# Kernel optimization log

Hardware: AMD Instinct MI355X
Metric: run time of the kernel (lower is better)

Reference implementation:

```python
import jax, jax.numpy as jnp
import numpy as np

H = 256   # d_model (SSM copies)
N = 32    # half state size (conjugate symmetry)
S = 256   # n_ssm (trainable copies); repeat = H//S = 1
R = 1     # low-rank correction rank
CCH = 32  # channels; must equal N for the final dC contraction
LMAX = 2048
BATCH = 2


def _r2c(x):
    return x[..., 0] + 1j * x[..., 1]


def setup_inputs() -> dict:
    key = jax.random.key(0)
    ks = jax.random.split(key, 8)
    # dt ~ loguniform(1e-3, 1e-1), standard S4 init
    log_dt = jnp.log(1e-3) + jax.random.uniform(ks[0], (H,), dtype=jnp.float32) * (jnp.log(1e-1) - jnp.log(1e-3))
    B_ri = 0.5 * jax.random.normal(ks[1], (1, S, N, 2), dtype=jnp.float32)
    P_ri = 0.5 * jax.random.normal(ks[2], (R, S, N, 2), dtype=jnp.float32)
    C_ri = 0.5 * jax.random.normal(ks[3], (CCH, H, N, 2), dtype=jnp.float32)
    # real_type='exp': w_real = -exp(inv_w_real) < 0 (stable poles)
    inv_w_real = 0.5 * jax.random.normal(ks[4], (S, N), dtype=jnp.float32)
    # HiPPO-style imaginary parts ~ pi * n, with small noise
    w_imag = jnp.pi * jnp.broadcast_to(jnp.arange(N, dtype=jnp.float32), (S, N)) + 0.01 * jax.random.normal(ks[5], (S, N), dtype=jnp.float32)
    dC = 0.1 * jax.random.normal(ks[6], (LMAX, H, N), dtype=jnp.float32)
    previous_decode = jax.random.normal(ks[7], (BATCH, H, LMAX), dtype=jnp.float32)
    return dict(log_dt=log_dt, B_ri=B_ri, P_ri=P_ri, C_ri=C_ri,
                inv_w_real=inv_w_real, w_imag=w_imag, dC=dC,
                previous_decode=previous_decode, L=LMAX)


def _ss_kernel(log_dt, B_ri, P_ri, C_ri, inv_w_real, w_imag, L):
    """NPLR SSM kernel K_L via Cauchy evaluation + rank-1 Woodbury + irfft. Returns (channels, H, L) real."""
    H_ = log_dt.shape[0]
    S_ = inv_w_real.shape[0]
    rep = H_ // S_
    dt = jnp.exp(log_dt)                              # (H,)
    B = _r2c(B_ri)                                    # (1, S, N)
    P = _r2c(P_ri)                                    # (R, S, N)
    C = _r2c(C_ri)                                    # (CCH, H, N)
    Q = jnp.conj(P)
    w = -jnp.exp(inv_w_real) + 1j * w_imag            # (S, N), real_type='exp'
    # FFT nodes (roots of unity) and bilinear-transformed nodes
    Lf = L // 2 + 1
    omega = jnp.exp((-2j * jnp.pi / L) * jnp.arange(Lf, dtype=jnp.float32))  # (Lf,)
    z = 2 * (1 - omega) / (1 + omega)                 # (Lf,)
    # broadcast S -> H ('r t n -> r (v t) n')
    B = jnp.tile(B, (1, rep, 1))                      # (1, H, N)
    P = jnp.tile(P, (1, rep, 1))                      # (R, H, N)
    Q = jnp.tile(Q, (1, rep, 1))
    w = jnp.tile(w, (rep, 1)) * dt[:, None]           # (H, N) : w * dt
    Bc = jnp.concatenate([B, P], axis=0)              # (1+R, H, N)
    Cc = jnp.concatenate([C, Q], axis=0)              # (CCH+R, H, N)
    v = Bc[:, None] * Cc[None]                        # (1+R, CCH+R, H, N)
    # conjugate-symmetric Cauchy kernel: sum_n v/(z-w) + conj(v)/(z-conj(w))
    cau_p = 1.0 / (z[None, None, :] - w[:, :, None])              # (H, N, Lf)
    cau_m = 1.0 / (z[None, None, :] - jnp.conj(w)[:, :, None])    # (H, N, Lf)
    r = jnp.einsum('ijhn,hnl->ijhl', v, cau_p) + jnp.einsum('ijhn,hnl->ijhl', jnp.conj(v), cau_m)
    r = r * dt[None, None, :, None]
    # rank-1 Woodbury correction
    k_f = r[:-1, :-1] - r[:-1, -1:] * r[-1:, :-1] / (1 + r[-1:, -1:])  # (1, CCH, H, Lf)
    k_f = k_f * 2 / (1 + omega)
    k = jnp.fft.irfft(k_f, n=L, axis=-1)              # (1, CCH, H, L) real
    return k[-1]                                      # (CCH, H, L)


def reference(log_dt, B_ri, P_ri, C_ri, inv_w_real, w_imag, dC, previous_decode, L):
    k = _ss_kernel(log_dt, B_ri, P_ri, C_ri, inv_w_real, w_imag, L)  # (CCH, H, L)
    # FFT convolution of previous_decode with the kernel (length-2L, linear conv)
    k_f = jnp.fft.rfft(k, n=2 * L, axis=-1)                          # (CCH, H, L+1)
    pd_f = jnp.fft.rfft(previous_decode, n=2 * L, axis=-1)           # (B, H, L+1)
    x_f = jnp.einsum('bhl,chl->bhcl', pd_f, k_f)                     # (B, H, CCH, L+1)
    x_pred = jnp.fft.irfft(x_f, n=2 * L, axis=-1)[..., :L]           # (B, H, CCH, L)
    out = jnp.einsum('bhnl,lhn->bhl', x_pred, dC)                    # (B, H, L)
    return out
```

## Files before the change

### kernel.cpp

```cpp
#include <hip/hip_runtime.h>
#include <math.h>

#define LF   1025

#define OFF_ZT   65536
#define OFF_KF   131072
#define OFF_PDF  67371008
#define OFF_DCT  84148224

__device__ __forceinline__ float2 cmulf(float2 a, float2 b){
    return make_float2(a.x*b.x - a.y*b.y, a.x*b.y + a.y*b.x);
}
__device__ __forceinline__ int pidx(int i){ return i + (i >> 4); }

__device__ __forceinline__ float2 twid(float r){
    float s, c;
    asm("v_sin_f32 %0, %1" : "=v"(s) : "v"(r));
    asm("v_cos_f32 %0, %1" : "=v"(c) : "v"(r));
    return make_float2(c, -s);
}

__global__ void initk(float4* __restrict__ ZT){
    int i = blockIdx.x*256 + threadIdx.x;
    if (i < LF){
        double th = (-2.0*M_PI) * (double)i / 2048.0;
        double cr = cos(th), ci = sin(th);
        double ar = 1.0 + cr, ai = ci;
        double den = ar*ar + ai*ai;
        double nr = 1.0 - cr, ni = -ci;
        double zr = 2.0*(nr*ar + ni*ai)/den;
        double zi = 2.0*(ni*ar - nr*ai)/den;
        ZT[i] = make_float4((float)zr, (float)zi, (float)(2.0*ar/den), (float)(-2.0*ai/den));
    }
}

__global__ void transpose_dC(const float* __restrict__ dC, float* __restrict__ DCT){
    __shared__ float tile[32][33];
    int hc0 = blockIdx.x*32;
    int l0  = blockIdx.y*32;
    int tx = threadIdx.x;
    for (int i = threadIdx.y; i < 32; i += 8)
        tile[i][tx] = dC[(size_t)(l0+i)*8192 + hc0 + tx];
    __syncthreads();
    for (int i = threadIdx.y; i < 32; i += 8)
        DCT[(size_t)(hc0+i)*2048 + l0 + tx] = tile[tx][i];
}

__global__ __launch_bounds__(256) void cauchy_k(
                         const float* __restrict__ log_dt, const float* __restrict__ B_ri,
                         const float* __restrict__ P_ri, const float* __restrict__ C_ri,
                         const float* __restrict__ ivw, const float* __restrict__ wimag,
                         const float4* __restrict__ ZT, float2* __restrict__ KF)
{
    const int h  = blockIdx.y;
    const int c0 = blockIdx.z * 8;
    const int l  = blockIdx.x*256 + (int)threadIdx.x;
    __shared__ float wre[32], wim[32], bre[32], bim[32], ppre[32], ppim[32];
    __shared__ float cre[8][32], cim[8][32];
    __shared__ float dt_sh;
    if (threadIdx.x < 32){
        int n = threadIdx.x;
        float dt = expf(log_dt[h]);
        wre[n] = -expf(ivw[h*32+n]) * dt;
        wim[n] = wimag[h*32+n] * dt;
        bre[n] = B_ri[(h*32+n)*2+0];
        bim[n] = B_ri[(h*32+n)*2+1];
        ppre[n] = P_ri[(h*32+n)*2+0];
        ppim[n] = P_ri[(h*32+n)*2+1];
        if (n == 0) dt_sh = dt;
    }
    {
        int i = threadIdx.x;
        int cc = i >> 5, n = i & 31;
        size_t base = (((size_t)(c0+cc)*256 + h)*32 + n)*2;
        cre[cc][n] = C_ri[base+0];
        cim[cc][n] = C_ri[base+1];
    }
    __syncthreads();
    if (l >= LF) return;

    float4 zt = ZT[l];
    const float zx = zt.x, zy = zt.y;
    float r0x[9], r0y[9], r1x[9], r1y[9];
    #pragma unroll
    for (int j=0;j<9;++j){ r0x[j]=0.f; r0y[j]=0.f; r1x[j]=0.f; r1y[j]=0.f; }

    #pragma unroll 1
    for (int n=0; n<32; ++n){
        float wr = wre[n], wi = wim[n];
        float dx = zx - wr;
        float dy = zy - wi;
        float ey = zy + wi;
        float ip = 1.0f/(dx*dx + dy*dy);
        float im = 1.0f/(dx*dx + ey*ey);
        float cpx = dx*ip, cpy = -dy*ip;
        float cmx = dx*im, cmy = -ey*im;
        float br = bre[n], bi = bim[n];
        float t0x = br*cpx - bi*cpy, t0y = br*cpy + bi*cpx;
        float t1x = br*cmx + bi*cmy, t1y = br*cmy - bi*cmx;
        float pr = ppre[n], pi = ppim[n];
        float t2x = pr*cpx - pi*cpy, t2y = pr*cpy + pi*cpx;
        float t3x = pr*cmx + pi*cmy, t3y = pr*cmy - pi*cmx;
        float u0 = t0x+t1x, v0 = t1y-t0y, s0 = t0y+t1y, q0 = t0x-t1x;
        float u1 = t2x+t3x, v1 = t3y-t2y, s1 = t2y+t3y, q1 = t2x-t3x;
        #pragma unroll
        for (int j=0;j<8;++j){
            float a = cre[j][n], b = cim[j][n];
            r0x[j] = fmaf(a,u0, fmaf(b,v0, r0x[j]));
            r0y[j] = fmaf(a,s0, fmaf(b,q0, r0y[j]));
            r1x[j] = fmaf(a,u1, fmaf(b,v1, r1x[j]));
            r1y[j] = fmaf(a,s1, fmaf(b,q1, r1y[j]));
        }
        r0x[8] = fmaf(pr,u0, fmaf(-pi,v0, r0x[8]));
        r0y[8] = fmaf(pr,s0, fmaf(-pi,q0, r0y[8]));
        r1x[8] = fmaf(pr,u1, fmaf(-pi,v1, r1x[8]));
        r1y[8] = fmaf(pr,s1, fmaf(-pi,q1, r1y[8]));
    }

    float dt = dt_sh;
    #pragma unroll
    for (int j=0;j<9;++j){ r0x[j]*=dt; r0y[j]*=dt; r1x[j]*=dt; r1y[j]*=dt; }
    float drr = 1.0f + r1x[8], dii = r1y[8];
    float idn = 1.0f/(drr*drr + dii*dii);
    float gx = (r0x[8]*drr + r0y[8]*dii)*idn;
    float gy = (r0y[8]*drr - r0x[8]*dii)*idn;
    float tfx = zt.z, tfy = zt.w;
    #pragma unroll
    for (int j=0;j<8;++j){
        float kr = r0x[j] - (gx*r1x[j] - gy*r1y[j]);
        float ki = r0y[j] - (gx*r1y[j] + gy*r1x[j]);
        KF[((size_t)((c0+j)*256+h))*1026 + l] = make_float2(kr*tfx - ki*tfy, kr*tfy + ki*tfx);
    }
}

template<bool INV>
__device__ __forceinline__ void bfly8(float2 v[8]){
    float2 e0,e1,e2,e3,o0,o1,o2,o3;
    {
        float t0x=v[0].x+v[4].x, t0y=v[0].y+v[4].y;
        float t1x=v[0].x-v[4].x, t1y=v[0].y-v[4].y;
        float t2x=v[2].x+v[6].x, t2y=v[2].y+v[6].y;
        float t3x=v[2].x-v[6].x, t3y=v[2].y-v[6].y;
        e0 = make_float2(t0x+t2x, t0y+t2y);
        e2 = make_float2(t0x-t2x, t0y-t2y);
        if (!INV){ e1 = make_float2(t1x+t3y, t1y-t3x); e3 = make_float2(t1x-t3y, t1y+t3x); }
        else     { e1 = make_float2(t1x-t3y, t1y+t3x); e3 = make_float2(t1x+t3y, t1y-t3x); }
    }
    {
        float t0x=v[1].x+v[5].x, t0y=v[1].y+v[5].y;
        float t1x=v[1].x-v[5].x, t1y=v[1].y-v[5].y;
        float t2x=v[3].x+v[7].x, t2y=v[3].y+v[7].y;
        float t3x=v[3].x-v[7].x, t3y=v[3].y-v[7].y;
        o0 = make_float2(t0x+t2x, t0y+t2y);
        o2 = make_float2(t0x-t2x, t0y-t2y);
        if (!INV){ o1 = make_float2(t1x+t3y, t1y-t3x); o3 = make_float2(t1x-t3y, t1y+t3x); }
        else     { o1 = make_float2(t1x-t3y, t1y+t3x); o3 = make_float2(t1x+t3y, t1y-t3x); }
    }
    const float RC = 0.70710678118654752f;
    float2 w1o1, w2o2, w3o3;
    if (!INV){
        w1o1 = make_float2(RC*(o1.x+o1.y), RC*(o1.y-o1.x));
        w2o2 = make_float2(o2.y, -o2.x);
        w3o3 = make_float2(RC*(o3.y-o3.x), RC*(-o3.x-o3.y));
    } else {
        w1o1 = make_float2(RC*(o1.x-o1.y), RC*(o1.y+o1.x));
        w2o2 = make_float2(-o2.y, o2.x);
        w3o3 = make_float2(RC*(-o3.x-o3.y), RC*(o3.x-o3.y));
    }
    v[0] = make_float2(e0.x+o0.x,   e0.y+o0.y);
    v[1] = make_float2(e1.x+w1o1.x, e1.y+w1o1.y);
    v[2] = make_float2(e2.x+w2o2.x, e2.y+w2o2.y);
    v[3] = make_float2(e3.x+w3o3.x, e3.y+w3o3.y);
    v[4] = make_float2(e0.x-o0.x,   e0.y-o0.y);
    v[5] = make_float2(e1.x-w1o1.x, e1.y-w1o1.y);
    v[6] = make_float2(e2.x-w2o2.x, e2.y-w2o2.y);
    v[7] = make_float2(e3.x-w3o3.x, e3.y-w3o3.y);
}

template<bool INV>
__device__ __forceinline__ void s1_reg8(float2 v[8], float2* __restrict__ out){
    bfly8<INV>(v);
    int d = (int)threadIdx.x << 3;
    #pragma unroll
    for (int q=0;q<8;++q) out[pidx(d+q)] = v[q];
}

template<bool INV, int NS>
__device__ __forceinline__ void r8stage(const float2* __restrict__ in, float2* __restrict__ out){
    __syncthreads();
    int j = (int)threadIdx.x;
    int jm = j & (NS-1);
    float2 v[8];
    #pragma unroll
    for (int m=0;m<8;++m) v[m] = in[pidx(j + m*256)];
    {
        const float SC = (float)(4096/(NS*8)) * (1.0f/4096.0f);
        float rb = (float)jm * SC;
        #pragma unroll
        for (int m=1;m<8;++m){
            float2 w = twid((float)m * rb);
            if (INV) w.y = -w.y;
            v[m] = cmulf(v[m], w);
        }
    }
    bfly8<INV>(v);
    int d = ((j - jm) << 3) + jm;
    #pragma unroll
    for (int q=0;q<8;++q) out[pidx(d + q*NS)] = v[q];
}

template<bool INV, int NS>
__device__ __forceinline__ void r4stage(const float2* __restrict__ in, float2* __restrict__ out){
    __syncthreads();
    #pragma unroll
    for (int it=0; it<2; ++it){
        int j = (int)threadIdx.x + it*256;
        int jm = j & (NS-1);
        float2 v0 = in[pidx(j)];
        float2 v1 = in[pidx(j +  512)];
        float2 v2 = in[pidx(j + 1024)];
        float2 v3 = in[pidx(j + 1536)];
        const float SC = (float)(4096/(NS*4)) * (1.0f/4096.0f);
        float rb = (float)jm * SC;
        float2 w1 = twid(rb), w2 = twid(2.0f*rb), w3 = twid(3.0f*rb);
        if (INV){ w1.y=-w1.y; w2.y=-w2.y; w3.y=-w3.y; }
        v1 = cmulf(v1,w1); v2 = cmulf(v2,w2); v3 = cmulf(v3,w3);
        float t0x=v0.x+v2.x, t0y=v0.y+v2.y;
        float t1x=v0.x-v2.x, t1y=v0.y-v2.y;
        float t2x=v1.x+v3.x, t2y=v1.y+v3.y;
        float t3x=v1.x-v3.x, t3y=v1.y-v3.y;
        float2 x0 = make_float2(t0x+t2x, t0y+t2y);
        float2 x2 = make_float2(t0x-t2x, t0y-t2y);
        float2 x1, x3;
        if (!INV){ x1 = make_float2(t1x+t3y, t1y-t3x); x3 = make_float2(t1x-t3y, t1y+t3x); }
        else     { x1 = make_float2(t1x-t3y, t1y+t3x); x3 = make_float2(t1x+t3y, t1y-t3x); }
        int d = ((j - jm) << 2) + jm;
        out[pidx(d)] = x0; out[pidx(d+NS)] = x1; out[pidx(d+2*NS)] = x2; out[pidx(d+3*NS)] = x3;
    }
}

template<bool INV>
__device__ __forceinline__ void fftR(float2 v[8], float2* __restrict__ A, float2* __restrict__ B){
    s1_reg8<INV>(v, A);
    r8stage<INV,8  >(A,B);
    r8stage<INV,64 >(B,A);
    r4stage<INV,512>(A,B);
    __syncthreads();
}

__global__ __launch_bounds__(256,2) void kernC2(const float* __restrict__ pd,
                                                float2* __restrict__ PDE, float2* __restrict__ PDO){
    __shared__ float2 A[2176], Bb[2176];
    const int t = threadIdx.x;
    const int h = blockIdx.x;
    const float* p0 = pd + (size_t)h * 2048;
    const float* p1 = pd + (size_t)(256 + h) * 2048;
    float2 z[8], v[8];
    #pragma unroll
    for (int m=0;m<8;++m){
        int j = t + m*256;
        z[m] = make_float2(p0[j], p1[j]);
        v[m] = z[m];
    }
    fftR<false>(v, A, Bb);
    float2* oe = PDE + (size_t)h * 2048;
    #pragma unroll
    for (int m=0;m<8;++m){ int j = t + m*256; oe[j] = Bb[pidx(j)]; }
    #pragma unroll
    for (int m=0;m<8;++m){
        int j = t + m*256;
        v[m] = cmulf(twid((float)j * (1.0f/4096.0f)), z[m]);
    }
    fftR<false>(v, A, Bb);
    float2* oo = PDO + (size_t)h * 2048;
    #pragma unroll
    for (int m=0;m<8;++m){ int j = t + m*256; oo[j] = Bb[pidx(j)]; }
}

__global__ __launch_bounds__(256,2) void kernF(const float2* __restrict__ KFb,
                                               const float2* __restrict__ PDE,
                                               const float2* __restrict__ PDO,
                                               const float* __restrict__ DCT,
                                               float* __restrict__ out){
    __shared__ float2 A[2176], Bb[2176];
    __shared__ float2 pde_s[2048], pdo_s[2048];
    const int t = threadIdx.x;
    const int h = blockIdx.x;
    const int cq = blockIdx.y;
    {
        const float2* pe = PDE + (size_t)h * 2048;
        const float2* po = PDO + (size_t)h * 2048;
        #pragma unroll
        for (int m=0;m<8;++m){
            int j = t + m*256;
            pde_s[j] = pe[j];
            pdo_s[j] = po[j];
        }
    }
    float accr[8], acci[8];
    #pragma unroll
    for (int m=0;m<8;++m){ accr[m]=0.f; acci[m]=0.f; }
    __syncthreads();

    #pragma unroll 1
    for (int pp=0; pp<8; ++pp){
        const int ca = cq*16 + pp*2;
        const float2* ra = KFb + (size_t)(ca*256+h)*1026;
        const float2* rb = KFb + (size_t)((ca+1)*256+h)*1026;

        float dcva[8], dcvb[8];
        {
            const float* dcta = DCT + (size_t)(h*32 + ca) * 2048;
            const float* dctb = dcta + 2048;
            #pragma unroll
            for (int m=0;m<8;++m){
                int j = t + m*256;
                dcva[m] = dcta[j] * (1.0f/4096.0f);
                dcvb[m] = dctb[j] * (1.0f/4096.0f);
            }
        }
        float2 v[8];

        #pragma unroll
        for (int m=0;m<8;++m){
            int j = t + m*256;
            float2 u;
            if (j <= 1024) u = ra[j];
            else { float2 w = ra[2048-j]; u = make_float2(w.x, -w.y); }
            v[m] = cmulf(pde_s[j], u);
        }
        fftR<true>(v, A, Bb);
        #pragma unroll
        for (int m=0;m<8;++m){
            int j = t + m*256;
            float2 xe = Bb[pidx(j)];
            accr[m] = fmaf(xe.x, dcva[m], accr[m]);
            acci[m] = fmaf(xe.y, dcva[m], acci[m]);
        }
        #pragma unroll
        for (int m=0;m<8;++m){
            int j = t + m*256;
            float2 u;
            if (j <= 1024) u = rb[j];
            else { float2 w = rb[2048-j]; u = make_float2(w.x, -w.y); }
            v[m] = cmulf(pde_s[j], u);
        }
        fftR<true>(v, A, Bb);
        #pragma unroll
        for (int m=0;m<8;++m){
            int j = t + m*256;
            float2 xe = Bb[pidx(j)];
            accr[m] = fmaf(xe.x, dcvb[m], accr[m]);
            acci[m] = fmaf(xe.y, dcvb[m], acci[m]);
        }

        #pragma unroll
        for (int m=0;m<8;++m){
            int j = t + m*256;
            float2 va, vb;
            if (j <= 1024){ va = ra[j]; vb = rb[j]; }
            else {
                float2 u = ra[2048-j]; va = make_float2(u.x, -u.y);
                float2 w = rb[2048-j]; vb = make_float2(w.x, -w.y);
            }
            v[m] = make_float2(va.x - vb.y, va.y + vb.x);
        }
        fftR<true>(v, A, Bb);
        #pragma unroll
        for (int m=0;m<8;++m){
            int j = t + m*256;
            float2 kk = Bb[pidx(j)];
            kk.x *= (1.0f/2048.0f); kk.y *= (1.0f/2048.0f);
            v[m] = cmulf(kk, twid((float)j * (1.0f/4096.0f)));
        }
        fftR<false>(v, A, Bb);

        float2 pa[8], sb[8];
        #pragma unroll
        for (int m=0;m<8;++m){
            int j  = t + m*256;
            int jm2 = 2047 - j;
            float2 z  = Bb[pidx(j)];
            float2 zm = Bb[pidx(jm2)];
            float2 Ka = make_float2(0.5f*(z.x + zm.x), 0.5f*(z.y - zm.y));
            float2 Kb = make_float2(0.5f*(z.y + zm.y), 0.5f*(zm.x - z.x));
            float2 pov = pdo_s[j];
            pa[m] = cmulf(pov, Ka);
            sb[m] = cmulf(pov, Kb);
        }
        fftR<true>(pa, A, Bb);
        #pragma unroll
        for (int m=0;m<8;++m){
            int j = t + m*256;
            float2 w = twid((float)j * (1.0f/4096.0f));
            float2 ee = make_float2(w.x, -w.y);
            float2 rot = cmulf(ee, Bb[pidx(j)]);
            accr[m] = fmaf(rot.x, dcva[m], accr[m]);
            acci[m] = fmaf(rot.y, dcva[m], acci[m]);
        }
        fftR<true>(sb, A, Bb);
        #pragma unroll
        for (int m=0;m<8;++m){
            int j = t + m*256;
            float2 w = twid((float)j * (1.0f/4096.0f));
            float2 ee = make_float2(w.x, -w.y);
            float2 rot = cmulf(ee, Bb[pidx(j)]);
            accr[m] = fmaf(rot.x, dcvb[m], accr[m]);
            acci[m] = fmaf(rot.y, dcvb[m], acci[m]);
        }
    }
    #pragma unroll
    for (int m=0;m<8;++m){
        int j = t + m*256;
        atomicAdd(&out[((size_t)h)*2048 + j],       accr[m]);
        atomicAdd(&out[((size_t)(256+h))*2048 + j], acci[m]);
    }
}

extern "C" void kernel_launch(void* const* d_in, const int* in_sizes, int n_in,
                              void* d_out, int out_size, void* d_ws, size_t ws_size,
                              hipStream_t stream) {
    const float* log_dt = (const float*)d_in[0];
    const float* B_ri   = (const float*)d_in[1];
    const float* P_ri   = (const float*)d_in[2];
    const float* C_ri   = (const float*)d_in[3];
    const float* ivw    = (const float*)d_in[4];
    const float* wimag  = (const float*)d_in[5];
    const float* dC     = (const float*)d_in[6];
    const float* pd     = (const float*)d_in[7];

    char* ws = (char*)d_ws;
    float4* ZT  = (float4*)(ws + OFF_ZT);
    float2* KF  = (float2*)(ws + OFF_KF);
    float2* PDE = (float2*)(ws + OFF_PDF);
    float2* PDO = (float2*)(ws + OFF_PDF + 256*2048*sizeof(float2));
    float*  DCT = (float*) (ws + OFF_DCT);
    float* out = (float*)d_out;

    hipMemsetAsync(out, 0, (size_t)out_size * sizeof(float), stream);
    initk<<<5, 256, 0, stream>>>(ZT);
    transpose_dC<<<dim3(256,64), dim3(32,8), 0, stream>>>(dC, DCT);
    cauchy_k<<<dim3(5,256,4), 256, 0, stream>>>(log_dt, B_ri, P_ri, C_ri, ivw, wimag, ZT, KF);
    kernC2<<<256, 256, 0, stream>>>(pd, PDE, PDO);
    kernF<<<dim3(256,2), 256, 0, stream>>>((const float2*)KF, PDE, PDO, DCT, out);
}
```

Baseline: 439.8 us.

## Restructure 2048-point FFT as radix-4 split into per-wavefront 512-point FFTs

Replaces the radix-8/8/8/4 shared-memory FFT with a first radix-4 decimation stage followed by four independent 512-point sub-FFTs, each owned by one 64-thread wavefront. The middle stages then need only an LDS wait instead of block-wide barriers, and twiddle powers are built by repeated complex multiplies rather than separate sin/cos calls. Output ends up in a bin-permuted padded layout, so every consumer index changes to a slot mapping. Exact divisions in the Cauchy kernel are also swapped for the hardware reciprocal instruction, at some precision cost.

```diff
diff --git a/kernel.cpp b/kernel.cpp
--- a/kernel.cpp
+++ b/kernel.cpp
@@ -11,7 +11,6 @@
 __device__ __forceinline__ float2 cmulf(float2 a, float2 b){
     return make_float2(a.x*b.x - a.y*b.y, a.x*b.y + a.y*b.x);
 }
-__device__ __forceinline__ int pidx(int i){ return i + (i >> 4); }
 
 __device__ __forceinline__ float2 twid(float r){
     float s, c;
@@ -19,6 +18,16 @@
     asm("v_cos_f32 %0, %1" : "=v"(c) : "v"(r));
     return make_float2(c, -s);
 }
+__device__ __forceinline__ float frcp(float x){
+    float y; asm("v_rcp_f32 %0, %1" : "=v"(y) : "v"(x)); return y;
+}
+__device__ __forceinline__ void lds_fence(){
+    asm volatile("s_waitcnt lgkmcnt(0)" ::: "memory");
+}
+
+#define GS 548
+__device__ __forceinline__ int gslot(int g, int s){ return g*GS + s + (s >> 4); }
+__device__ __forceinline__ int binslot(int j){ return gslot(j & 3, j >> 2); }
 
 __global__ void initk(float4* __restrict__ ZT){
     int i = blockIdx.x*256 + threadIdx.x;
@@ -91,8 +100,8 @@
         float dx = zx - wr;
         float dy = zy - wi;
         float ey = zy + wi;
-        float ip = 1.0f/(dx*dx + dy*dy);
-        float im = 1.0f/(dx*dx + ey*ey);
+        float ip = frcp(dx*dx + dy*dy);
+        float im = frcp(dx*dx + ey*ey);
         float cpx = dx*ip, cpy = -dy*ip;
         float cmx = dx*im, cmy = -ey*im;
         float br = bre[n], bi = bim[n];
@@ -121,7 +130,7 @@
     #pragma unroll
     for (int j=0;j<9;++j){ r0x[j]*=dt; r0y[j]*=dt; r1x[j]*=dt; r1y[j]*=dt; }
     float drr = 1.0f + r1x[8], dii = r1y[8];
-    float idn = 1.0f/(drr*drr + dii*dii);
+    float idn = frcp(drr*drr + dii*dii);
     float gx = (r0x[8]*drr + r0y[8]*dii)*idn;
     float gy = (r0y[8]*drr - r0x[8]*dii)*idn;
     float tfx = zt.z, tfy = zt.w;
@@ -178,79 +187,76 @@
 }
 
 template<bool INV>
-__device__ __forceinline__ void s1_reg8(float2 v[8], float2* __restrict__ out){
-    bfly8<INV>(v);
-    int d = (int)threadIdx.x << 3;
-    #pragma unroll
-    for (int q=0;q<8;++q) out[pidx(d+q)] = v[q];
-}
-
-template<bool INV, int NS>
-__device__ __forceinline__ void r8stage(const float2* __restrict__ in, float2* __restrict__ out){
+__device__ __forceinline__ void fftR(float2 v[8], float2* __restrict__ A, float2* __restrict__ B){
+    const int t = threadIdx.x;
+    #pragma unroll
+    for (int half=0; half<2; ++half){
+        int r = t + half*256;
+        float2 x0=v[half], x1=v[2+half], x2=v[4+half], x3=v[6+half];
+        float t0x=x0.x+x2.x, t0y=x0.y+x2.y;
+        float t1x=x0.x-x2.x, t1y=x0.y-x2.y;
+        float t2x=x1.x+x3.x, t2y=x1.y+x3.y;
+        float t3x=x1.x-x3.x, t3y=x1.y-x3.y;
+        float2 y0 = make_float2(t0x+t2x, t0y+t2y);
+        float2 y2 = make_float2(t0x-t2x, t0y-t2y);
+        float2 y1, y3;
+        if (!INV){ y1 = make_float2(t1x+t3y, t1y-t3x); y3 = make_float2(t1x-t3y, t1y+t3x); }
+        else     { y1 = make_float2(t1x-t3y, t1y+t3x); y3 = make_float2(t1x+t3y, t1y-t3x); }
+        float2 w1 = twid((float)r * (1.0f/2048.0f));
+        if (INV) w1.y = -w1.y;
+        float2 w2 = cmulf(w1,w1);
+        float2 w3 = cmulf(w2,w1);
+        A[gslot(0,r)] = y0;
+        A[gslot(1,r)] = cmulf(y1,w1);
+        A[gslot(2,r)] = cmulf(y2,w2);
+        A[gslot(3,r)] = cmulf(y3,w3);
+    }
     __syncthreads();
-    int j = (int)threadIdx.x;
-    int jm = j & (NS-1);
-    float2 v[8];
-    #pragma unroll
-    for (int m=0;m<8;++m) v[m] = in[pidx(j + m*256)];
-    {
-        const float SC = (float)(4096/(NS*8)) * (1.0f/4096.0f);
-        float rb = (float)jm * SC;
-        #pragma unroll
-        for (int m=1;m<8;++m){
-            float2 w = twid((float)m * rb);
-            if (INV) w.y = -w.y;
-            v[m] = cmulf(v[m], w);
-        }
-    }
-    bfly8<INV>(v);
-    int d = ((j - jm) << 3) + jm;
-    #pragma unroll
-    for (int q=0;q<8;++q) out[pidx(d + q*NS)] = v[q];
-}
-
-template<bool INV, int NS>
-__device__ __forceinline__ void r4stage(const float2* __restrict__ in, float2* __restrict__ out){
-    __syncthreads();
-    #pragma unroll
-    for (int it=0; it<2; ++it){
-        int j = (int)threadIdx.x + it*256;
-        int jm = j & (NS-1);
-        float2 v0 = in[pidx(j)];
-        float2 v1 = in[pidx(j +  512)];
-        float2 v2 = in[pidx(j + 1024)];
-        float2 v3 = in[pidx(j + 1536)];
-        const float SC = (float)(4096/(NS*4)) * (1.0f/4096.0f);
-        float rb = (float)jm * SC;
-        float2 w1 = twid(rb), w2 = twid(2.0f*rb), w3 = twid(3.0f*rb);
-        if (INV){ w1.y=-w1.y; w2.y=-w2.y; w3.y=-w3.y; }
-        v1 = cmulf(v1,w1); v2 = cmulf(v2,w2); v3 = cmulf(v3,w3);
-        float t0x=v0.x+v2.x, t0y=v0.y+v2.y;
-        float t1x=v0.x-v2.x, t1y=v0.y-v2.y;
-        float t2x=v1.x+v3.x, t2y=v1.y+v3.y;
-        float t3x=v1.x-v3.x, t3y=v1.y-v3.y;
-        float2 x0 = make_float2(t0x+t2x, t0y+t2y);
-        float2 x2 = make_float2(t0x-t2x, t0y-t2y);
-        float2 x1, x3;
-        if (!INV){ x1 = make_float2(t1x+t3y, t1y-t3x); x3 = make_float2(t1x-t3y, t1y+t3x); }
-        else     { x1 = make_float2(t1x-t3y, t1y+t3x); x3 = make_float2(t1x+t3y, t1y-t3x); }
-        int d = ((j - jm) << 2) + jm;
-        out[pidx(d)] = x0; out[pidx(d+NS)] = x1; out[pidx(d+2*NS)] = x2; out[pidx(d+3*NS)] = x3;
-    }
-}
-
-template<bool INV>
-__device__ __forceinline__ void fftR(float2 v[8], float2* __restrict__ A, float2* __restrict__ B){
-    s1_reg8<INV>(v, A);
-    r8stage<INV,8  >(A,B);
-    r8stage<INV,64 >(B,A);
-    r4stage<INV,512>(A,B);
+    const int w = t >> 6, l = t & 63;
+    {
+        float2 u[8];
+        #pragma unroll
+        for (int m=0;m<8;++m) u[m] = A[gslot(w, l + 64*m)];
+        bfly8<INV>(u);
+        #pragma unroll
+        for (int q=0;q<8;++q) B[gslot(w, 8*l+q)] = u[q];
+    }
+    lds_fence();
+    {
+        float2 u[8];
+        #pragma unroll
+        for (int m=0;m<8;++m) u[m] = B[gslot(w, l + 64*m)];
+        int jm = l & 7;
+        float2 w1 = twid((float)jm * (1.0f/64.0f));
+        if (INV) w1.y = -w1.y;
+        float2 wc = w1;
+        #pragma unroll
+        for (int m=1;m<8;++m){ u[m] = cmulf(u[m], wc); if (m<7) wc = cmulf(wc, w1); }
+        bfly8<INV>(u);
+        int d = ((l - jm) << 3) + jm;
+        #pragma unroll
+        for (int q=0;q<8;++q) A[gslot(w, d + q*8)] = u[q];
+    }
+    lds_fence();
+    {
+        float2 u[8];
+        #pragma unroll
+        for (int m=0;m<8;++m) u[m] = A[gslot(w, l + 64*m)];
+        float2 w1 = twid((float)l * (1.0f/512.0f));
+        if (INV) w1.y = -w1.y;
+        float2 wc = w1;
+        #pragma unroll
+        for (int m=1;m<8;++m){ u[m] = cmulf(u[m], wc); if (m<7) wc = cmulf(wc, w1); }
+        bfly8<INV>(u);
+        #pragma unroll
+        for (int q=0;q<8;++q) B[gslot(w, l + q*64)] = u[q];
+    }
     __syncthreads();
 }
 
 __global__ __launch_bounds__(256,2) void kernC2(const float* __restrict__ pd,
                                                 float2* __restrict__ PDE, float2* __restrict__ PDO){
-    __shared__ float2 A[2176], Bb[2176];
+    __shared__ float2 A[4*GS], Bb[4*GS];
     const int t = threadIdx.x;
     const int h = blockIdx.x;
     const float* p0 = pd + (size_t)h * 2048;
@@ -265,7 +271,7 @@
     fftR<false>(v, A, Bb);
     float2* oe = PDE + (size_t)h * 2048;
     #pragma unroll
-    for (int m=0;m<8;++m){ int j = t + m*256; oe[j] = Bb[pidx(j)]; }
+    for (int m=0;m<8;++m){ int j = t + m*256; oe[j] = Bb[binslot(j)]; }
     #pragma unroll
     for (int m=0;m<8;++m){
         int j = t + m*256;
@@ -274,7 +280,7 @@
     fftR<false>(v, A, Bb);
     float2* oo = PDO + (size_t)h * 2048;
     #pragma unroll
-    for (int m=0;m<8;++m){ int j = t + m*256; oo[j] = Bb[pidx(j)]; }
+    for (int m=0;m<8;++m){ int j = t + m*256; oo[j] = Bb[binslot(j)]; }
 }
 
 __global__ __launch_bounds__(256,2) void kernF(const float2* __restrict__ KFb,
@@ -282,7 +288,7 @@
                                                const float2* __restrict__ PDO,
                                                const float* __restrict__ DCT,
                                                float* __restrict__ out){
-    __shared__ float2 A[2176], Bb[2176];
+    __shared__ float2 A[4*GS], Bb[4*GS];
     __shared__ float2 pde_s[2048], pdo_s[2048];
     const int t = threadIdx.x;
     const int h = blockIdx.x;
@@ -333,7 +339,7 @@
         #pragma unroll
         for (int m=0;m<8;++m){
             int j = t + m*256;
-            float2 xe = Bb[pidx(j)];
+            float2 xe = Bb[binslot(j)];
             accr[m] = fmaf(xe.x, dcva[m], accr[m]);
             acci[m] = fmaf(xe.y, dcva[m], acci[m]);
         }
@@ -349,7 +355,7 @@
         #pragma unroll
         for (int m=0;m<8;++m){
             int j = t + m*256;
-            float2 xe = Bb[pidx(j)];
+            float2 xe = Bb[binslot(j)];
             accr[m] = fmaf(xe.x, dcvb[m], accr[m]);
             acci[m] = fmaf(xe.y, dcvb[m], acci[m]);
         }
@@ -369,7 +375,7 @@
         #pragma unroll
         for (int m=0;m<8;++m){
             int j = t + m*256;
-            float2 kk = Bb[pidx(j)];
+            float2 kk = Bb[binslot(j)];
             kk.x *= (1.0f/2048.0f); kk.y *= (1.0f/2048.0f);
             v[m] = cmulf(kk, twid((float)j * (1.0f/4096.0f)));
         }
@@ -379,9 +385,8 @@
         #pragma unroll
         for (int m=0;m<8;++m){
             int j  = t + m*256;
-            int jm2 = 2047 - j;
-            float2 z  = Bb[pidx(j)];
-            float2 zm = Bb[pidx(jm2)];
+            float2 z  = Bb[binslot(j)];
+            float2 zm = Bb[binslot(2047 - j)];
             float2 Ka = make_float2(0.5f*(z.x + zm.x), 0.5f*(z.y - zm.y));
             float2 Kb = make_float2(0.5f*(z.y + zm.y), 0.5f*(zm.x - z.x));
             float2 pov = pdo_s[j];
@@ -394,7 +399,7 @@
             int j = t + m*256;
             float2 w = twid((float)j * (1.0f/4096.0f));
             float2 ee = make_float2(w.x, -w.y);
-            float2 rot = cmulf(ee, Bb[pidx(j)]);
+            float2 rot = cmulf(ee, Bb[binslot(j)]);
             accr[m] = fmaf(rot.x, dcva[m], accr[m]);
             acci[m] = fmaf(rot.y, dcva[m], acci[m]);
         }
@@ -404,7 +409,7 @@
             int j = t + m*256;
             float2 w = twid((float)j * (1.0f/4096.0f));
             float2 ee = make_float2(w.x, -w.y);
-            float2 rot = cmulf(ee, Bb[pidx(j)]);
+            float2 rot = cmulf(ee, Bb[binslot(j)]);
             accr[m] = fmaf(rot.x, dcvb[m], accr[m]);
             acci[m] = fmaf(rot.y, dcvb[m], acci[m]);
         }
```

After: 364.8 us. -17.1%, faster.
